# Performance work log

Measured on AMD Instinct MI355X. Metric: run time of the kernel, lower is better.

Reference implementation:

```python
import jax, jax.numpy as jnp
import numpy as np

BLOCK_SIZES = [256] * 8            # sum = N_CTX = 2048
B, H, D = 2, 16, 64
N_CTX = sum(BLOCK_SIZES)
SPARSITY_PATTERN = 'block_causal'  # row_starts = 0, row_ends = end of own block


def _build_masks(block_sizes, pattern):
    cs = np.cumsum([0] + list(block_sizes))
    row_ends = np.concatenate([np.full(bs, cs[i + 1], dtype=np.int32)
                               for i, bs in enumerate(block_sizes)])
    if pattern == 'block_diagonal':
        row_starts = np.concatenate([np.full(bs, cs[i], dtype=np.int32)
                                     for i, bs in enumerate(block_sizes)])
    elif pattern == 'block_causal':
        row_starts = np.zeros_like(row_ends)
    else:
        raise ValueError(pattern)
    return jnp.asarray(row_starts), jnp.asarray(row_ends)


def setup_inputs() -> dict:
    key = jax.random.key(0)
    kq, kk, kv = jax.random.split(key, 3)
    q = jax.random.normal(kq, (B, H, N_CTX, D), dtype=jnp.float32)
    k = jax.random.normal(kk, (B, H, N_CTX, D), dtype=jnp.float32)
    v = jax.random.normal(kv, (B, H, N_CTX, D), dtype=jnp.float32)
    row_starts, row_ends = _build_masks(BLOCK_SIZES, SPARSITY_PATTERN)
    sm_scale = jnp.float32(1.0 / np.sqrt(D))
    return {"q": q, "k": k, "v": v, "sm_scale": sm_scale,
            "row_starts": row_starts, "row_ends": row_ends}


def reference(q, k, v, sm_scale, row_starts, row_ends):
    # q,k,v: [B,H,N,D]; per query row i, attend to kv cols in [row_starts[i], row_ends[i])
    n = q.shape[2]
    cols = jnp.arange(n, dtype=jnp.int32)
    allowed = (cols[None, :] >= row_starts[:, None]) & (cols[None, :] < row_ends[:, None])  # [N,N]
    scores = jnp.einsum('bhqd,bhkd->bhqk', q, k) * sm_scale
    neg = jnp.finfo(scores.dtype).min
    scores = jnp.where(allowed[None, None], scores, neg)
    p = jax.nn.softmax(scores, axis=-1)
    return jnp.einsum('bhqk,bhkd->bhqd', p, v)
```

## Files before the change

### kernel.cpp

```cpp
#include <hip/hip_runtime.h>


typedef short bf16x8 __attribute__((ext_vector_type(8)));
typedef float f32x4  __attribute__((ext_vector_type(4)));
typedef unsigned short u16;
typedef u16 u16x8 __attribute__((ext_vector_type(8)));

#define MFMA(A,B,C) __builtin_amdgcn_mfma_f32_16x16x32_bf16((A),(B),(C),0,0,0)

__device__ __forceinline__ u16 f2bf_rne(float f) {
    union { float f; unsigned u; } c; c.f = f;
    unsigned r = c.u + 0x7FFFu + ((c.u >> 16) & 1u);
    return (u16)(r >> 16);
}
__device__ __forceinline__ u16 f2bf_fast(float f) {
    union { float f; unsigned u; } c; c.f = f;
    return (u16)((c.u + 0x8000u) >> 16);
}

__global__ __launch_bounds__(256)
void prep_kernel(const float* __restrict__ K, const float* __restrict__ V,
                 u16* __restrict__ blob)
{
    int bt = blockIdx.x;
    int tid = threadIdx.x;
    const size_t gbase = (size_t)bt * 4096;
    u16* bb = blob + (size_t)bt * 8192;
    __shared__ __align__(16) u16 lt[4096];

    int key = tid >> 2;
    int c2  = (tid & 3) << 1;
    int rotb = (key & 3) + 4 * ((key >> 3) & 1);
    {
        const float* kp = K + gbase + key * 64 + c2 * 8;
        float4 x0 = *(const float4*)kp,       x1 = *(const float4*)(kp + 4);
        float4 x2 = *(const float4*)(kp + 8), x3 = *(const float4*)(kp + 12);
        u16x8 a, b;
        a[0]=f2bf_rne(x0.x); a[1]=f2bf_rne(x0.y); a[2]=f2bf_rne(x0.z); a[3]=f2bf_rne(x0.w);
        a[4]=f2bf_rne(x1.x); a[5]=f2bf_rne(x1.y); a[6]=f2bf_rne(x1.z); a[7]=f2bf_rne(x1.w);
        b[0]=f2bf_rne(x2.x); b[1]=f2bf_rne(x2.y); b[2]=f2bf_rne(x2.z); b[3]=f2bf_rne(x2.w);
        b[4]=f2bf_rne(x3.x); b[5]=f2bf_rne(x3.y); b[6]=f2bf_rne(x3.z); b[7]=f2bf_rne(x3.w);
        *(u16x8*)&bb[key * 64 + (((c2    ) + rotb) & 7) * 8] = a;
        *(u16x8*)&bb[key * 64 + (((c2 + 1) + rotb) & 7) * 8] = b;
    }
    {
        const float* vp = V + gbase + key * 64 + c2 * 8;
        float4 y0 = *(const float4*)vp,       y1 = *(const float4*)(vp + 4);
        float4 y2 = *(const float4*)(vp + 8), y3 = *(const float4*)(vp + 12);
        float yy[16] = { y0.x,y0.y,y0.z,y0.w, y1.x,y1.y,y1.z,y1.w,
                         y2.x,y2.y,y2.z,y2.w, y3.x,y3.y,y3.z,y3.w };
        int kc = key >> 3, kw = key & 7;
        #pragma unroll
        for (int j = 0; j < 16; ++j) {
            int d = c2 * 8 + j;
            lt[d * 64 + ((kc + (d & 7)) & 7) * 8 + kw] = f2bf_rne(yy[j]);
        }
    }
    __syncthreads();
    {
        int o = tid * 16;
        *(u16x8*)&bb[4096 + o]     = *(const u16x8*)&lt[o];
        *(u16x8*)&bb[4096 + o + 8] = *(const u16x8*)&lt[o + 8];
    }
}

__global__ __launch_bounds__(256, 4)
void bsattn_main(const float* __restrict__ Q, const float* __restrict__ SC,
                 const int* __restrict__ RS, const int* __restrict__ RE,
                 const u16* __restrict__ blob, float* __restrict__ O)
{
    constexpr int N = 2048, D = 64;
    int wg = blockIdx.x;
    int bh = wg & 31, qt = wg >> 5;
    int q0 = qt << 6;
    int tid = threadIdx.x, wid = tid >> 6, lane = tid & 63;
    int n = lane & 15, g = lane >> 4;

    __shared__ __align__(16) u16 lsm[16384];
    __shared__ int sb[4][2];

    int myrow = q0 + wid * 16 + n;
    int rs_l = RS[myrow], re_l = RE[myrow];
    int w_rs_min = rs_l, w_rs_max = rs_l, w_re_min = re_l, w_re_max = re_l;
    #pragma unroll
    for (int o = 1; o < 16; o <<= 1) {
        w_rs_min = min(w_rs_min, __shfl_xor(w_rs_min, o));
        w_rs_max = max(w_rs_max, __shfl_xor(w_rs_max, o));
        w_re_min = min(w_re_min, __shfl_xor(w_re_min, o));
        w_re_max = max(w_re_max, __shfl_xor(w_re_max, o));
    }
    if (lane == 0) { sb[wid][0] = w_rs_min; sb[wid][1] = w_re_max; }

    float sscale = SC[0] * 1.44269504088896340736f;

    bf16x8 qf0, qf1;
    {
        const float* qp = Q + ((size_t)bh * N + myrow) * D + g * 8;
        float4 a0 = *(const float4*)qp,        a1 = *(const float4*)(qp + 4);
        float4 b0 = *(const float4*)(qp + 32), b1 = *(const float4*)(qp + 36);
        qf0[0]=f2bf_rne(a0.x*sscale); qf0[1]=f2bf_rne(a0.y*sscale);
        qf0[2]=f2bf_rne(a0.z*sscale); qf0[3]=f2bf_rne(a0.w*sscale);
        qf0[4]=f2bf_rne(a1.x*sscale); qf0[5]=f2bf_rne(a1.y*sscale);
        qf0[6]=f2bf_rne(a1.z*sscale); qf0[7]=f2bf_rne(a1.w*sscale);
        qf1[0]=f2bf_rne(b0.x*sscale); qf1[1]=f2bf_rne(b0.y*sscale);
        qf1[2]=f2bf_rne(b0.z*sscale); qf1[3]=f2bf_rne(b0.w*sscale);
        qf1[4]=f2bf_rne(b1.x*sscale); qf1[5]=f2bf_rne(b1.y*sscale);
        qf1[6]=f2bf_rne(b1.z*sscale); qf1[7]=f2bf_rne(b1.w*sscale);
    }

    __syncthreads();
    int kst  = min(min(sb[0][0], sb[1][0]), min(sb[2][0], sb[3][0])) & ~63;
    int kend = max(max(sb[0][1], sb[1][1]), max(sb[2][1], sb[3][1]));

    int rA  = ((n >> 2) << 3) + (n & 3);
    int phk = (n & 3) + 4 * ((n >> 2) & 1);
    int osA0 = rA * 64 + ((g     + phk) & 7) * 8;
    int osA1 = rA * 64 + ((g + 4 + phk) & 7) * 8;
    int ov0 = 4096 + n * 64 + ((    g + (n & 7)) & 7) * 8;
    int ov1 = 4096 + n * 64 + ((4 + g + (n & 7)) & 7) * 8;

    f32x4 acc[4], accl = {0.f, 0.f, 0.f, 0.f};
    #pragma unroll
    for (int c = 0; c < 4; ++c) acc[c] = (f32x4){0.f, 0.f, 0.f, 0.f};
    bf16x8 ones;
    #pragma unroll
    for (int j = 0; j < 8; ++j) ones[j] = (short)0x3F80;

    auto proc = [&](int kb, const u16* ls) {
        float sc[16];
        #pragma unroll
        for (int h = 0; h < 2; ++h) {
            int hb = h * 2048;
            f32x4 t0 = {0.f,0.f,0.f,0.f}, t1 = t0;
            t0 = MFMA(*(const bf16x8*)&ls[hb + osA0],       qf0, t0);
            t0 = MFMA(*(const bf16x8*)&ls[hb + osA1],       qf1, t0);
            t1 = MFMA(*(const bf16x8*)&ls[hb + osA0 + 256], qf0, t1);
            t1 = MFMA(*(const bf16x8*)&ls[hb + osA1 + 256], qf1, t1);
            #pragma unroll
            for (int r = 0; r < 4; ++r) { sc[h*8 + r] = t0[r]; sc[h*8 + 4 + r] = t1[r]; }
        }
        if (kb < w_rs_max || kb + 64 > w_re_min) {
            #pragma unroll
            for (int h = 0; h < 2; ++h)
                #pragma unroll
                for (int j = 0; j < 8; ++j) {
                    int key = kb + h * 32 + g * 8 + j;
                    if (key < rs_l || key >= re_l) sc[h*8 + j] = -1e30f;
                }
        }
        bf16x8 pf0, pf1;
        #pragma unroll
        for (int j = 0; j < 8; ++j) { float p = __builtin_amdgcn_exp2f(sc[j]);     pf0[j] = (short)f2bf_fast(p); }
        #pragma unroll
        for (int j = 0; j < 8; ++j) { float p = __builtin_amdgcn_exp2f(sc[8 + j]); pf1[j] = (short)f2bf_fast(p); }
        #pragma unroll
        for (int h = 0; h < 2; ++h) {
            const bf16x8& pf = h ? pf1 : pf0;
            int ov = h ? ov1 : ov0;
            acc[0] = MFMA(pf, *(const bf16x8*)&ls[ov       ], acc[0]);
            acc[1] = MFMA(pf, *(const bf16x8*)&ls[ov + 1024], acc[1]);
            acc[2] = MFMA(pf, *(const bf16x8*)&ls[ov + 2048], acc[2]);
            acc[3] = MFMA(pf, *(const bf16x8*)&ls[ov + 3072], acc[3]);
            accl   = MFMA(pf, ones, accl);
        }
    };

    for (int kt = kst; kt < kend; kt += 128) {
        __syncthreads();
        bool two = (kt + 64) < kend;
        const u16* src = blob + ((size_t)(bh * 32) + (kt >> 6)) * 8192;
        int cnt = two ? 4 : 2;
        #pragma unroll
        for (int i = 0; i < 4; ++i) {
            if (i < cnt) {
                int o = i * 4096 + tid * 16;
                *(u16x8*)&lsm[o]     = *(const u16x8*)&src[o];
                *(u16x8*)&lsm[o + 8] = *(const u16x8*)&src[o + 8];
            }
        }
        __syncthreads();
        if (kt < w_re_max && kt + 64 > w_rs_min)
            proc(kt, lsm);
        if (two && (kt + 64) < w_re_max && kt + 128 > w_rs_min)
            proc(kt + 64, lsm + 8192);
    }

    int rb = g << 2;
    int orow = q0 + wid * 16 + rb;
    float* ob = O + ((size_t)bh * N + orow) * D + n;
    #pragma unroll
    for (int r = 0; r < 4; ++r) {
        float li = 1.0f / accl[r];
        float* rp = ob + (size_t)r * D;
        rp[0]  = acc[0][r] * li;
        rp[16] = acc[1][r] * li;
        rp[32] = acc[2][r] * li;
        rp[48] = acc[3][r] * li;
    }
}

extern "C" void kernel_launch(void* const* d_in, const int* in_sizes, int n_in,
                              void* d_out, int out_size, void* d_ws, size_t ws_size,
                              hipStream_t stream) {
    const float* q  = (const float*)d_in[0];
    const float* k  = (const float*)d_in[1];
    const float* v  = (const float*)d_in[2];
    const float* sc = (const float*)d_in[3];
    const int* rs   = (const int*)d_in[4];
    const int* re   = (const int*)d_in[5];
    float* out      = (float*)d_out;
    u16* blob       = (u16*)d_ws;

    prep_kernel<<<dim3(1024), dim3(256), 0, stream>>>(k, v, blob);
    bsattn_main<<<dim3(1024), dim3(256), 0, stream>>>(q, sc, rs, re, blob, out);
}
```

Measured before the change: 135.4 us.

## Pair heavy and light query tiles per block with split-KV load balancing

```diff
diff --git a/kernel.cpp b/kernel.cpp
--- a/kernel.cpp
+++ b/kernel.cpp
@@ -28,10 +28,9 @@
     u16* bb = blob + (size_t)bt * 8192;
     __shared__ __align__(16) u16 lt[4096];
 
-    int key = tid >> 2;
-    int c2  = (tid & 3) << 1;
-    int rotb = (key & 3) + 4 * ((key >> 3) & 1);
     {
+        int key = tid >> 2, c2 = (tid & 3) << 1;
+        int rotb = (key & 3) + 4 * ((key >> 3) & 1);
         const float* kp = K + gbase + key * 64 + c2 * 8;
         float4 x0 = *(const float4*)kp,       x1 = *(const float4*)(kp + 4);
         float4 x2 = *(const float4*)(kp + 8), x3 = *(const float4*)(kp + 12);
@@ -44,16 +43,17 @@
         *(u16x8*)&bb[key * 64 + (((c2 + 1) + rotb) & 7) * 8] = b;
     }
     {
-        const float* vp = V + gbase + key * 64 + c2 * 8;
+        int wv = tid >> 6, ln = tid & 63;
+        const float* vp = V + gbase + ln * 64 + wv * 16;
         float4 y0 = *(const float4*)vp,       y1 = *(const float4*)(vp + 4);
         float4 y2 = *(const float4*)(vp + 8), y3 = *(const float4*)(vp + 12);
         float yy[16] = { y0.x,y0.y,y0.z,y0.w, y1.x,y1.y,y1.z,y1.w,
                          y2.x,y2.y,y2.z,y2.w, y3.x,y3.y,y3.z,y3.w };
-        int kc = key >> 3, kw = key & 7;
+        int kc = ln >> 3, kw = ln & 7;
         #pragma unroll
         for (int j = 0; j < 16; ++j) {
-            int d = c2 * 8 + j;
-            lt[d * 64 + ((kc + (d & 7)) & 7) * 8 + kw] = f2bf_rne(yy[j]);
+            int d = wv * 16 + j;
+            lt[d * 64 + ((kc + (j & 7)) & 7) * 8 + kw] = f2bf_rne(yy[j]);
         }
     }
     __syncthreads();
@@ -64,38 +64,48 @@
     }
 }
 
-__global__ __launch_bounds__(256, 4)
+__global__ __launch_bounds__(512, 4)
 void bsattn_main(const float* __restrict__ Q, const float* __restrict__ SC,
                  const int* __restrict__ RS, const int* __restrict__ RE,
                  const u16* __restrict__ blob, float* __restrict__ O)
 {
     constexpr int N = 2048, D = 64;
     int wg = blockIdx.x;
-    int bh = wg & 31, qt = wg >> 5;
-    int q0 = qt << 6;
-    int tid = threadIdx.x, wid = tid >> 6, lane = tid & 63;
+    int bh = wg & 31, pr = wg >> 5;
+    int qtA = 31 - pr, qtB = pr;
+    int tid = threadIdx.x;
+    int grp = tid >> 8;
+    int wid = (tid >> 6) & 3;
+    int lane = tid & 63;
     int n = lane & 15, g = lane >> 4;
 
-    __shared__ __align__(16) u16 lsm[16384];
-    __shared__ int sb[4][2];
-
-    int myrow = q0 + wid * 16 + n;
+    __shared__ __align__(16) unsigned char smem[33280];
+    u16*   buf0 = (u16*)smem;
+    u16*   buf1 = (u16*)(smem + 16384);
+    float* cmb  = (float*)smem;
+    float* cl   = (float*)(smem + 32768);
+    int*   sbi  = (int*)(smem + 33024);
+
+    int myqt  = grp ? qtB : qtA;
+    int myrow = (myqt << 6) + wid * 16 + n;
     int rs_l = RS[myrow], re_l = RE[myrow];
-    int w_rs_min = rs_l, w_rs_max = rs_l, w_re_min = re_l, w_re_max = re_l;
-    #pragma unroll
-    for (int o = 1; o < 16; o <<= 1) {
-        w_rs_min = min(w_rs_min, __shfl_xor(w_rs_min, o));
-        w_rs_max = max(w_rs_max, __shfl_xor(w_rs_max, o));
-        w_re_min = min(w_re_min, __shfl_xor(w_re_min, o));
-        w_re_max = max(w_re_max, __shfl_xor(w_re_max, o));
-    }
-    if (lane == 0) { sb[wid][0] = w_rs_min; sb[wid][1] = w_re_max; }
-
+    {
+        int a = rs_l, b = rs_l, c = re_l, d = re_l;
+        #pragma unroll
+        for (int o = 1; o < 16; o <<= 1) {
+            a = min(a, __shfl_xor(a, o)); b = max(b, __shfl_xor(b, o));
+            c = min(c, __shfl_xor(c, o)); d = max(d, __shfl_xor(d, o));
+        }
+        if (lane == 0) {
+            int* p = &sbi[(grp * 4 + wid) * 4];
+            p[0] = a; p[1] = b; p[2] = c; p[3] = d;
+        }
+    }
     float sscale = SC[0] * 1.44269504088896340736f;
 
     bf16x8 qf0, qf1;
-    {
-        const float* qp = Q + ((size_t)bh * N + myrow) * D + g * 8;
+    auto loadQ = [&](int row) {
+        const float* qp = Q + ((size_t)bh * N + row) * D + g * 8;
         float4 a0 = *(const float4*)qp,        a1 = *(const float4*)(qp + 4);
         float4 b0 = *(const float4*)(qp + 32), b1 = *(const float4*)(qp + 36);
         qf0[0]=f2bf_rne(a0.x*sscale); qf0[1]=f2bf_rne(a0.y*sscale);
@@ -106,18 +116,29 @@
         qf1[2]=f2bf_rne(b0.z*sscale); qf1[3]=f2bf_rne(b0.w*sscale);
         qf1[4]=f2bf_rne(b1.x*sscale); qf1[5]=f2bf_rne(b1.y*sscale);
         qf1[6]=f2bf_rne(b1.z*sscale); qf1[7]=f2bf_rne(b1.w*sscale);
-    }
+    };
+    loadQ(myrow);
 
     __syncthreads();
-    int kst  = min(min(sb[0][0], sb[1][0]), min(sb[2][0], sb[3][0])) & ~63;
-    int kend = max(max(sb[0][1], sb[1][1]), max(sb[2][1], sb[3][1]));
-
-    int rA  = ((n >> 2) << 3) + (n & 3);
-    int phk = (n & 3) + 4 * ((n >> 2) & 1);
-    int osA0 = rA * 64 + ((g     + phk) & 7) * 8;
-    int osA1 = rA * 64 + ((g + 4 + phk) & 7) * 8;
-    int ov0 = 4096 + n * 64 + ((    g + (n & 7)) & 7) * 8;
-    int ov1 = 4096 + n * 64 + ((4 + g + (n & 7)) & 7) * 8;
+    int rsminA = min(min(sbi[0],  sbi[4]),  min(sbi[8],  sbi[12]));
+    int rsmaxA = max(max(sbi[1],  sbi[5]),  max(sbi[9],  sbi[13]));
+    int reminA = min(min(sbi[2],  sbi[6]),  min(sbi[10], sbi[14]));
+    int remaxA = max(max(sbi[3],  sbi[7]),  max(sbi[11], sbi[15]));
+    int rsminB = min(min(sbi[16], sbi[20]), min(sbi[24], sbi[28]));
+    int rsmaxB = max(max(sbi[17], sbi[21]), max(sbi[25], sbi[29]));
+    int reminB = min(min(sbi[18], sbi[22]), min(sbi[26], sbi[30]));
+    int remaxB = max(max(sbi[19], sbi[23]), max(sbi[27], sbi[31]));
+
+    int sA = rsminA >> 6;
+    int wA = (remaxA - (sA << 6) + 63) >> 6;
+    int sB = rsminB >> 6;
+    int wB = (remaxB - (sB << 6) + 63) >> 6;
+    int n0 = (wA + wB + 1) >> 1; if (n0 > wA) n0 = wA;
+    int c1 = wB + wA - n0;
+    int M  = max(n0, c1);
+
+    int mk_rsmax = grp ? rsmaxB : rsmaxA;
+    int mk_remin = grp ? reminB : reminA;
 
     f32x4 acc[4], accl = {0.f, 0.f, 0.f, 0.f};
     #pragma unroll
@@ -125,6 +146,13 @@
     bf16x8 ones;
     #pragma unroll
     for (int j = 0; j < 8; ++j) ones[j] = (short)0x3F80;
+
+    int rA   = ((n >> 2) << 3) + (n & 3);
+    int phk  = (n & 3) + 4 * ((n >> 2) & 1);
+    int osA0 = rA * 64 + ((g + phk) & 7) * 8;
+    int osA1 = rA * 64 + ((g + 4 + phk) & 7) * 8;
+    int ov0  = 4096 + n * 64 + ((    g + (n & 7)) & 7) * 8;
+    int ov1  = 4096 + n * 64 + ((4 + g + (n & 7)) & 7) * 8;
 
     auto proc = [&](int kb, const u16* ls) {
         float sc[16];
@@ -139,7 +167,7 @@
             #pragma unroll
             for (int r = 0; r < 4; ++r) { sc[h*8 + r] = t0[r]; sc[h*8 + 4 + r] = t1[r]; }
         }
-        if (kb < w_rs_max || kb + 64 > w_re_min) {
+        if (kb < mk_rsmax || kb + 64 > mk_remin) {
             #pragma unroll
             for (int h = 0; h < 2; ++h)
                 #pragma unroll
@@ -165,37 +193,94 @@
         }
     };
 
-    for (int kt = kst; kt < kend; kt += 128) {
+    auto epilogue = [&](int qt) {
+        int rb = g << 2;
+        int orow = (qt << 6) + wid * 16 + rb;
+        float* ob = O + ((size_t)bh * N + orow) * D + n;
+        #pragma unroll
+        for (int r = 0; r < 4; ++r) {
+            float li = 1.0f / accl[r];
+            float* rp = ob + (size_t)r * D;
+            rp[0]  = acc[0][r] * li;
+            rp[16] = acc[1][r] * li;
+            rp[32] = acc[2][r] * li;
+            rp[48] = acc[3][r] * li;
+        }
+    };
+
+    bool onB = (grp == 1);
+    for (int i = 0; i < M; ++i) {
+        int  tA = sA + i;
+        bool v0 = (i < n0);
+        int  j  = i - wB;
+        bool v1 = (i < wB) || (j < wA - n0);
+        int  tBt = (i < wB) ? (sB + i) : (sA + n0 + j);
+        bool sh = v0 && v1 && (tBt == tA);
         __syncthreads();
-        bool two = (kt + 64) < kend;
-        const u16* src = blob + ((size_t)(bh * 32) + (kt >> 6)) * 8192;
-        int cnt = two ? 4 : 2;
-        #pragma unroll
-        for (int i = 0; i < 4; ++i) {
-            if (i < cnt) {
-                int o = i * 4096 + tid * 16;
-                *(u16x8*)&lsm[o]     = *(const u16x8*)&src[o];
-                *(u16x8*)&lsm[o + 8] = *(const u16x8*)&src[o + 8];
+        if (grp == 0) {
+            if (v0) {
+                const u16* src = blob + (size_t)(bh * 32 + tA) * 8192;
+                int o = (tid & 255) * 32;
+                #pragma unroll
+                for (int q8 = 0; q8 < 4; ++q8)
+                    *(u16x8*)&buf0[o + q8 * 8] = *(const u16x8*)&src[o + q8 * 8];
             }
+        } else {
+            if (v1 && !sh) {
+                const u16* src = blob + (size_t)(bh * 32 + tBt) * 8192;
+                int o = (tid & 255) * 32;
+                #pragma unroll
+                for (int q8 = 0; q8 < 4; ++q8)
+                    *(u16x8*)&buf1[o + q8 * 8] = *(const u16x8*)&src[o + q8 * 8];
+            }
         }
         __syncthreads();
-        if (kt < w_re_max && kt + 64 > w_rs_min)
-            proc(kt, lsm);
-        if (two && (kt + 64) < w_re_max && kt + 128 > w_rs_min)
-            proc(kt + 64, lsm + 8192);
-    }
-
-    int rb = g << 2;
-    int orow = q0 + wid * 16 + rb;
-    float* ob = O + ((size_t)bh * N + orow) * D + n;
-    #pragma unroll
-    for (int r = 0; r < 4; ++r) {
-        float li = 1.0f / accl[r];
-        float* rp = ob + (size_t)r * D;
-        rp[0]  = acc[0][r] * li;
-        rp[16] = acc[1][r] * li;
-        rp[32] = acc[2][r] * li;
-        rp[48] = acc[3][r] * li;
+        if (grp == 0) {
+            if (v0) proc(tA << 6, buf0);
+        } else {
+            if (onB && i == wB) {
+                if (wB > 0) epilogue(qtB);
+                myrow = (qtA << 6) + wid * 16 + n;
+                rs_l = RS[myrow]; re_l = RE[myrow];
+                mk_rsmax = rsmaxA; mk_remin = reminA;
+                loadQ(myrow);
+                #pragma unroll
+                for (int c = 0; c < 4; ++c) acc[c] = (f32x4){0.f, 0.f, 0.f, 0.f};
+                accl = (f32x4){0.f, 0.f, 0.f, 0.f};
+                onB = false;
+            }
+            if (v1) proc(tBt << 6, sh ? buf0 : buf1);
+        }
+    }
+
+    __syncthreads();
+    if (grp == 1) {
+        if (onB) {
+            if (wB > 0) epilogue(qtB);
+            #pragma unroll
+            for (int c = 0; c < 4; ++c) acc[c] = (f32x4){0.f, 0.f, 0.f, 0.f};
+            accl = (f32x4){0.f, 0.f, 0.f, 0.f};
+        }
+        #pragma unroll
+        for (int c = 0; c < 4; ++c)
+            #pragma unroll
+            for (int r = 0; r < 4; ++r)
+                cmb[(wid * 16 + g * 4 + r) * 64 + ((c * 16 + n) ^ (g * 8))] = acc[c][r];
+        if (n == 0) {
+            #pragma unroll
+            for (int r = 0; r < 4; ++r) cl[wid * 16 + g * 4 + r] = accl[r];
+        }
+    }
+    __syncthreads();
+    if (grp == 0) {
+        #pragma unroll
+        for (int c = 0; c < 4; ++c)
+            #pragma unroll
+            for (int r = 0; r < 4; ++r)
+                acc[c][r] += cmb[(wid * 16 + g * 4 + r) * 64 + ((c * 16 + n) ^ (g * 8))];
+        #pragma unroll
+        for (int r = 0; r < 4; ++r) accl[r] += cl[wid * 16 + g * 4 + r];
+        epilogue(qtA);
     }
 }
 
@@ -212,5 +297,5 @@
     u16* blob       = (u16*)d_ws;
 
     prep_kernel<<<dim3(1024), dim3(256), 0, stream>>>(k, v, blob);
-    bsattn_main<<<dim3(1024), dim3(256), 0, stream>>>(q, sc, rs, re, blob, out);
-}
+    bsattn_main<<<dim3(512), dim3(512), 0, stream>>>(q, sc, rs, re, blob, out);
+}
```

Measured after the change: 135.6 us. No clear change (+0.1%).

## Double-buffer K/V tiles via async global-to-LDS loads and reorder query tiles

Applied to the files above, without the earlier changes.

```diff
diff --git a/kernel.cpp b/kernel.cpp
--- a/kernel.cpp
+++ b/kernel.cpp
@@ -16,6 +16,12 @@
 __device__ __forceinline__ u16 f2bf_fast(float f) {
     union { float f; unsigned u; } c; c.f = f;
     return (u16)((c.u + 0x8000u) >> 16);
+}
+
+__device__ __forceinline__ void gload_lds16(const void* g, void* lds) {
+    __builtin_amdgcn_global_load_lds(
+        (const __attribute__((address_space(1))) unsigned int*)g,
+        (__attribute__((address_space(3))) unsigned int*)lds, 16, 0, 0);
 }
 
 __global__ __launch_bounds__(256)
@@ -27,11 +33,9 @@
     const size_t gbase = (size_t)bt * 4096;
     u16* bb = blob + (size_t)bt * 8192;
     __shared__ __align__(16) u16 lt[4096];
-
-    int key = tid >> 2;
-    int c2  = (tid & 3) << 1;
-    int rotb = (key & 3) + 4 * ((key >> 3) & 1);
-    {
+    {
+        int key = tid >> 2, c2 = (tid & 3) << 1;
+        int rotb = (key & 3) + 4 * ((key >> 3) & 1);
         const float* kp = K + gbase + key * 64 + c2 * 8;
         float4 x0 = *(const float4*)kp,       x1 = *(const float4*)(kp + 4);
         float4 x2 = *(const float4*)(kp + 8), x3 = *(const float4*)(kp + 12);
@@ -44,16 +48,17 @@
         *(u16x8*)&bb[key * 64 + (((c2 + 1) + rotb) & 7) * 8] = b;
     }
     {
-        const float* vp = V + gbase + key * 64 + c2 * 8;
+        int wv = tid >> 6, ln = tid & 63;
+        const float* vp = V + gbase + ln * 64 + wv * 16;
         float4 y0 = *(const float4*)vp,       y1 = *(const float4*)(vp + 4);
         float4 y2 = *(const float4*)(vp + 8), y3 = *(const float4*)(vp + 12);
         float yy[16] = { y0.x,y0.y,y0.z,y0.w, y1.x,y1.y,y1.z,y1.w,
                          y2.x,y2.y,y2.z,y2.w, y3.x,y3.y,y3.z,y3.w };
-        int kc = key >> 3, kw = key & 7;
+        int kc = ln >> 3, kw = ln & 7;
         #pragma unroll
         for (int j = 0; j < 16; ++j) {
-            int d = c2 * 8 + j;
-            lt[d * 64 + ((kc + (d & 7)) & 7) * 8 + kw] = f2bf_rne(yy[j]);
+            int d = wv * 16 + j;
+            lt[d * 64 + ((kc + (j & 7)) & 7) * 8 + kw] = f2bf_rne(yy[j]);
         }
     }
     __syncthreads();
@@ -71,13 +76,18 @@
 {
     constexpr int N = 2048, D = 64;
     int wg = blockIdx.x;
-    int bh = wg & 31, qt = wg >> 5;
+    int bh = wg & 31;
+    int i0 = wg >> 5, kk = i0 & 7, rr = i0 >> 3;
+    int qt = (rr == 0) ? ((kk < 4) ? 28 + kk : 20 + kk)
+           : (rr == 1) ? ((kk < 4) ? 20 + kk : 12 + kk)
+           : (rr == 2) ? (8 + kk) : kk;
     int q0 = qt << 6;
+
     int tid = threadIdx.x, wid = tid >> 6, lane = tid & 63;
     int n = lane & 15, g = lane >> 4;
 
     __shared__ __align__(16) u16 lsm[16384];
-    __shared__ int sb[4][2];
+    __shared__ int sbi[16];
 
     int myrow = q0 + wid * 16 + n;
     int rs_l = RS[myrow], re_l = RE[myrow];
@@ -89,7 +99,7 @@
         w_re_min = min(w_re_min, __shfl_xor(w_re_min, o));
         w_re_max = max(w_re_max, __shfl_xor(w_re_max, o));
     }
-    if (lane == 0) { sb[wid][0] = w_rs_min; sb[wid][1] = w_re_max; }
+    if (lane == 0) { sbi[wid * 2] = w_rs_min; sbi[wid * 2 + 1] = w_re_max; }
 
     float sscale = SC[0] * 1.44269504088896340736f;
 
@@ -109,15 +119,17 @@
     }
 
     __syncthreads();
-    int kst  = min(min(sb[0][0], sb[1][0]), min(sb[2][0], sb[3][0])) & ~63;
-    int kend = max(max(sb[0][1], sb[1][1]), max(sb[2][1], sb[3][1]));
-
-    int rA  = ((n >> 2) << 3) + (n & 3);
-    int phk = (n & 3) + 4 * ((n >> 2) & 1);
-    int osA0 = rA * 64 + ((g     + phk) & 7) * 8;
+    int kst  = min(min(sbi[0], sbi[2]), min(sbi[4], sbi[6])) & ~63;
+    int kend = max(max(sbi[1], sbi[3]), max(sbi[5], sbi[7]));
+    int t0 = kst >> 6;
+    int w  = (kend - kst + 63) >> 6;
+
+    int rA   = ((n >> 2) << 3) + (n & 3);
+    int phk  = (n & 3) + 4 * ((n >> 2) & 1);
+    int osA0 = rA * 64 + ((g + phk) & 7) * 8;
     int osA1 = rA * 64 + ((g + 4 + phk) & 7) * 8;
-    int ov0 = 4096 + n * 64 + ((    g + (n & 7)) & 7) * 8;
-    int ov1 = 4096 + n * 64 + ((4 + g + (n & 7)) & 7) * 8;
+    int ov0  = 4096 + n * 64 + ((    g + (n & 7)) & 7) * 8;
+    int ov1  = 4096 + n * 64 + ((4 + g + (n & 7)) & 7) * 8;
 
     f32x4 acc[4], accl = {0.f, 0.f, 0.f, 0.f};
     #pragma unroll
@@ -126,18 +138,29 @@
     #pragma unroll
     for (int j = 0; j < 8; ++j) ones[j] = (short)0x3F80;
 
+    auto stage = [&](int i) {
+        if (i < w) {
+            const u16* src = blob + (size_t)(bh * 32 + t0 + i) * 8192;
+            u16* dst = &lsm[(i & 1) << 13];
+            int wb = wid * 2048;
+            #pragma unroll
+            for (int c = 0; c < 4; ++c)
+                gload_lds16(src + wb + c * 512 + lane * 8, dst + wb + c * 512);
+        }
+    };
+
     auto proc = [&](int kb, const u16* ls) {
         float sc[16];
         #pragma unroll
         for (int h = 0; h < 2; ++h) {
             int hb = h * 2048;
-            f32x4 t0 = {0.f,0.f,0.f,0.f}, t1 = t0;
-            t0 = MFMA(*(const bf16x8*)&ls[hb + osA0],       qf0, t0);
-            t0 = MFMA(*(const bf16x8*)&ls[hb + osA1],       qf1, t0);
-            t1 = MFMA(*(const bf16x8*)&ls[hb + osA0 + 256], qf0, t1);
-            t1 = MFMA(*(const bf16x8*)&ls[hb + osA1 + 256], qf1, t1);
+            f32x4 t0v = {0.f,0.f,0.f,0.f}, t1v = t0v;
+            t0v = MFMA(*(const bf16x8*)&ls[hb + osA0],       qf0, t0v);
+            t0v = MFMA(*(const bf16x8*)&ls[hb + osA1],       qf1, t0v);
+            t1v = MFMA(*(const bf16x8*)&ls[hb + osA0 + 256], qf0, t1v);
+            t1v = MFMA(*(const bf16x8*)&ls[hb + osA1 + 256], qf1, t1v);
             #pragma unroll
-            for (int r = 0; r < 4; ++r) { sc[h*8 + r] = t0[r]; sc[h*8 + 4 + r] = t1[r]; }
+            for (int r = 0; r < 4; ++r) { sc[h*8 + r] = t0v[r]; sc[h*8 + 4 + r] = t1v[r]; }
         }
         if (kb < w_rs_max || kb + 64 > w_re_min) {
             #pragma unroll
@@ -165,24 +188,11 @@
         }
     };
 
-    for (int kt = kst; kt < kend; kt += 128) {
+    stage(0);
+    for (int i = 0; i < w; ++i) {
         __syncthreads();
-        bool two = (kt + 64) < kend;
-        const u16* src = blob + ((size_t)(bh * 32) + (kt >> 6)) * 8192;
-        int cnt = two ? 4 : 2;
-        #pragma unroll
-        for (int i = 0; i < 4; ++i) {
-            if (i < cnt) {
-                int o = i * 4096 + tid * 16;
-                *(u16x8*)&lsm[o]     = *(const u16x8*)&src[o];
-                *(u16x8*)&lsm[o + 8] = *(const u16x8*)&src[o + 8];
-            }
-        }
-        __syncthreads();
-        if (kt < w_re_max && kt + 64 > w_rs_min)
-            proc(kt, lsm);
-        if (two && (kt + 64) < w_re_max && kt + 128 > w_rs_min)
-            proc(kt + 64, lsm + 8192);
+        stage(i + 1);
+        proc(kst + (i << 6), &lsm[(i & 1) << 13]);
     }
 
     int rb = g << 2;
```

Result: faster. 131.4 us (-2.9%).
